# Kernel tuning notes

Hardware: AMD Instinct MI355X
Metric: run time of the kernel (lower is better)

## Reference

```python
import jax, jax.numpy as jnp
import numpy as np

B, N, C, H = 2, 2048, 1024, 16
D = C // H  # head_dim = 64

def setup_inputs() -> dict:
    key = jax.random.key(0)
    ks = jax.random.split(key, 8)
    x = jax.random.normal(ks[0], (B, N, C), jnp.float32)
    mask = jax.random.uniform(ks[1], (H, N, N), jnp.float32)
    gamma = jax.random.uniform(ks[2], (H,), jnp.float32)  # per-head decay in (0,1)
    state_prev = jax.random.normal(ks[3], (B, H, D, D), jnp.float32)
    w_scale = 0.02
    W_qkv = jax.random.normal(ks[4], (C, 3 * C), jnp.float32) * w_scale
    b_qkv = jnp.zeros((3 * C,), jnp.float32)
    W_out = jax.random.normal(ks[5], (C, C), jnp.float32) * w_scale
    b_out = jnp.zeros((C,), jnp.float32)
    return dict(x=x, mask=mask, gamma=gamma, state_prev=state_prev,
                W_qkv=W_qkv, b_qkv=b_qkv, W_out=W_out, b_out=b_out)

def reference(x, mask, gamma, state_prev, W_qkv, b_qkv, W_out, b_out):
    # Retention.chunkwise with state_prev (mode='chunkwise')
    b, n, c = x.shape
    h = gamma.shape[0]
    d = c // h
    scale = d ** -0.5
    qkv = (x @ W_qkv + b_qkv).reshape(b, n, 3, h, d)
    q = qkv[:, :, 0].transpose(0, 2, 1, 3) * scale  # [B,H,N,D]
    k = qkv[:, :, 1].transpose(0, 2, 1, 3)
    v = qkv[:, :, 2].transpose(0, 2, 1, 3)
    # intra-chunk decay-masked retention: [B,H,N,N]
    ret = jnp.einsum('bhnd,bhmd->bhnm', q, k) * mask
    ret = jnp.einsum('bhnm,bhmd->bhnd', ret, v)  # [B,H,N,D]
    inner_pos = jnp.arange(1, n + 1, dtype=x.dtype)  # [N], 1-based positions
    # state = sum_n gamma^(N-n) * k_n^T v_n (no [B,H,N,D,D] materialization)
    state_decays = gamma[:, None] ** (n - inner_pos)[None, :]  # [H,N]
    state = jnp.einsum('bhnd,bhne,hn->bhde', k, v, state_decays)  # [B,H,D,D]
    chunk_decay = gamma ** n  # [H]
    state = state + state_prev * chunk_decay[None, :, None, None]
    # cross-chunk retention against previous state
    cross = jnp.einsum('bhnd,bhde->bhne', q, state_prev)
    cross = cross * (gamma[None, :, None, None] ** inner_pos[None, None, :, None])
    ret = (ret + cross).transpose(0, 2, 1, 3).reshape(b, n, c)
    out = ret @ W_out + b_out
    return (out, state)
```

## Files before the change

kernel.cpp:

```cpp
#include <hip/hip_runtime.h>
#include <hip/hip_bf16.h>
#include <cstdint>

#define DI __device__ __forceinline__

typedef __attribute__((ext_vector_type(8))) short v8s;
typedef __attribute__((ext_vector_type(4))) float v4f;

constexpr int Bc = 2, Nc = 2048, Cc = 1024, Hc = 16, Dc = 64;

DI float bfbits(uint32_t u) { union { uint32_t i; float f; } c; c.i = u; return c.f; }
DI unsigned short f2bf(float f) {
    union { float f; uint32_t u; } c; c.f = f;
    uint32_t r = c.u + 0x7FFFu + ((c.u >> 16) & 1u);
    return (unsigned short)(r >> 16);
}
DI void unpackb8(uint4 u, float* f) {
    f[0] = bfbits(u.x << 16); f[1] = bfbits(u.x & 0xFFFF0000u);
    f[2] = bfbits(u.y << 16); f[3] = bfbits(u.y & 0xFFFF0000u);
    f[4] = bfbits(u.z << 16); f[5] = bfbits(u.z & 0xFFFF0000u);
    f[6] = bfbits(u.w << 16); f[7] = bfbits(u.w & 0xFFFF0000u);
}
DI float gpow(float g, float p) {
    if (p <= 0.f) return 1.f;
    if (g <= 0.f) return 0.f;
    return exp2f(p * log2f(g));
}

__global__ __launch_bounds__(256) void cvt_bf16(
    const float* __restrict__ in, unsigned short* __restrict__ out, int n8)
{
    int i = blockIdx.x * 256 + threadIdx.x;
    if (i >= n8) return;
    float4 a = ((const float4*)in)[i * 2];
    float4 b = ((const float4*)in)[i * 2 + 1];
    ushort4 r0; r0.x = f2bf(a.x); r0.y = f2bf(a.y); r0.z = f2bf(a.z); r0.w = f2bf(a.w);
    ushort4 r1; r1.x = f2bf(b.x); r1.y = f2bf(b.y); r1.z = f2bf(b.z); r1.w = f2bf(b.w);
    ((ushort4*)out)[i * 2] = r0; ((ushort4*)out)[i * 2 + 1] = r1;
}

__global__ __launch_bounds__(256) void transpose_cvt(
    const float* __restrict__ in, unsigned short* __restrict__ out, int R, int C)
{
    __shared__ float T[64][65];
    const int tid = threadIdx.x;
    const int r0 = blockIdx.y * 64, c0 = blockIdx.x * 64;
    #pragma unroll
    for (int rep = 0; rep < 4; rep++) {
        int row = (tid >> 4) + rep * 16, col = (tid & 15) * 4;
        float4 v = *reinterpret_cast<const float4*>(in + (size_t)(r0 + row) * C + c0 + col);
        T[row][col] = v.x; T[row][col + 1] = v.y; T[row][col + 2] = v.z; T[row][col + 3] = v.w;
    }
    __syncthreads();
    #pragma unroll
    for (int rep = 0; rep < 4; rep++) {
        int ocr = (tid >> 4) + rep * 16, j4 = (tid & 15) * 4;
        ushort4 w;
        w.x = f2bf(T[j4][ocr]);     w.y = f2bf(T[j4 + 1][ocr]);
        w.z = f2bf(T[j4 + 2][ocr]); w.w = f2bf(T[j4 + 3][ocr]);
        *reinterpret_cast<ushort4*>(out + (size_t)(c0 + ocr) * R + r0 + j4) = w;
    }
}

__global__ __launch_bounds__(256) void transpose_v(
    const unsigned short* __restrict__ in, unsigned short* __restrict__ out)
{
    __shared__ unsigned short T[64][72];
    const int tid = threadIdx.x;
    const int n0 = blockIdx.x * 64;
    const int bh = blockIdx.y;
    const unsigned short* src = in + ((size_t)bh * Nc + n0) * Dc;
    #pragma unroll
    for (int rep = 0; rep < 2; rep++) {
        int r = (tid >> 3) + rep * 32, c = (tid & 7) * 8;
        *(uint4*)&T[r][c] = *(const uint4*)(src + (size_t)r * Dc + c);
    }
    __syncthreads();
    unsigned short* dst = out + (size_t)bh * Dc * Nc + n0;
    #pragma unroll
    for (int rep = 0; rep < 2; rep++) {
        int d = (tid >> 3) + rep * 32, c0 = (tid & 7) * 8;
        union { uint4 u; unsigned short s[8]; } w;
        #pragma unroll
        for (int j = 0; j < 8; j++) w.s[j] = T[c0 + j][d];
        *(uint4*)(dst + (size_t)d * Nc + c0) = w.u;
    }
}

__global__ __launch_bounds__(256) void qkv_mfma(
    const unsigned short* __restrict__ A, const unsigned short* __restrict__ Bt,
    const float* __restrict__ bias,
    unsigned short* __restrict__ q, unsigned short* __restrict__ k,
    unsigned short* __restrict__ v)
{
    __shared__ unsigned short As[128][72];
    __shared__ unsigned short Bs[128][72];
    const int tid = threadIdx.x, wave = tid >> 6, lane = tid & 63;
    const int L = lane & 15, quad = lane >> 4;
    const int wr = (wave >> 1) * 64, wc = (wave & 1) * 64;
    const int row0 = blockIdx.y * 128, col0 = blockIdx.x * 128;
    v4f acc[4][4];
    #pragma unroll
    for (int i = 0; i < 4; i++)
        #pragma unroll
        for (int j = 0; j < 4; j++) { acc[i][j][0]=0.f; acc[i][j][1]=0.f; acc[i][j][2]=0.f; acc[i][j][3]=0.f; }
    for (int k0 = 0; k0 < 1024; k0 += 64) {
        __syncthreads();
        #pragma unroll
        for (int rep = 0; rep < 4; rep++) {
            int r = (tid >> 3) + rep * 32, cg = (tid & 7) * 8;
            *(uint4*)&As[r][cg] = *(const uint4*)(A  + (size_t)(row0 + r) * 1024 + k0 + cg);
            *(uint4*)&Bs[r][cg] = *(const uint4*)(Bt + (size_t)(col0 + r) * 1024 + k0 + cg);
        }
        __syncthreads();
        #pragma unroll
        for (int half = 0; half < 2; half++) {
            v8s af[4], bf[4];
            #pragma unroll
            for (int s = 0; s < 4; s++) {
                af[s] = *(v8s*)&As[wr + s * 16 + L][half * 32 + quad * 8];
                bf[s] = *(v8s*)&Bs[wc + s * 16 + L][half * 32 + quad * 8];
            }
            #pragma unroll
            for (int i = 0; i < 4; i++)
                #pragma unroll
                for (int j = 0; j < 4; j++)
                    acc[i][j] = __builtin_amdgcn_mfma_f32_16x16x32_bf16(af[i], bf[j], acc[i][j], 0, 0, 0);
        }
    }
    const int which = col0 >> 10;
    #pragma unroll
    for (int j = 0; j < 4; j++) {
        int c = col0 + wc + j * 16 + L;
        int h = (c & 1023) >> 6, d = c & 63;
        float bv = bias[c];
        #pragma unroll
        for (int i = 0; i < 4; i++) {
            #pragma unroll
            for (int reg = 0; reg < 4; reg++) {
                int rr = row0 + wr + i * 16 + quad * 4 + reg;
                int b = rr >> 11, n = rr & 2047;
                float val = acc[i][j][reg] + bv;
                size_t base = (((size_t)(b * Hc + h)) * Nc + n) * Dc + d;
                if (which == 0)      q[base] = f2bf(val * 0.125f);
                else if (which == 1) k[base] = f2bf(val);
                else                 v[base] = f2bf(val);
            }
        }
    }
}

__global__ __launch_bounds__(256, 4) void retention_mfma(
    const unsigned short* __restrict__ qb, const unsigned short* __restrict__ kb,
    const unsigned short* __restrict__ vtb,
    const float* __restrict__ mask, const float* __restrict__ gamma,
    const float* __restrict__ sprev,
    unsigned short* __restrict__ retb, float* __restrict__ pf0, float* __restrict__ pf1)
{
    __shared__ unsigned short Kt[64][72];
    __shared__ unsigned short Vt[64][72];
    __shared__ unsigned short Sm[64][72];
    const int tid = threadIdx.x, wave = tid >> 6, lane = tid & 63;
    const int L = lane & 15, quad = lane >> 4;
    const int h = blockIdx.y;
    const int n0 = blockIdx.x * 128;
    const int batch = blockIdx.z >> 1;
    const int chunk = blockIdx.z & 1;
    const int m_base = chunk * 1024;
    const float g = gamma[h];
    const int bh = batch * Hc + h;

    {
        #pragma unroll
        for (int rep = 0; rep < 2; rep++) {
            int r = (tid >> 3) + rep * 32, ch = (tid & 7) * 8;
            *(uint4*)&Kt[r][ch] = *(const uint4*)(qb + ((size_t)bh * Nc + n0 + r) * Dc + ch);
            *(uint4*)&Vt[r][ch] = *(const uint4*)(qb + ((size_t)bh * Nc + n0 + 64 + r) * Dc + ch);
        }
    }
    __syncthreads();
    v8s qf[2][2];
    qf[0][0] = *(v8s*)&Kt[wave * 16 + L][quad * 8];
    qf[0][1] = *(v8s*)&Kt[wave * 16 + L][32 + quad * 8];
    qf[1][0] = *(v8s*)&Vt[wave * 16 + L][quad * 8];
    qf[1][1] = *(v8s*)&Vt[wave * 16 + L][32 + quad * 8];

    v4f oacc[2][4];
    #pragma unroll
    for (int band = 0; band < 2; band++)
        #pragma unroll
        for (int s = 0; s < 4; s++) { oacc[band][s][0]=0.f; oacc[band][s][1]=0.f; oacc[band][s][2]=0.f; oacc[band][s][3]=0.f; }

    if (chunk == 0) {
        __syncthreads();
        {
            int dd = tid >> 2, e0 = (tid & 3) * 16;
            const float* sp = sprev + ((size_t)bh * 64 + dd) * 64 + e0;
            #pragma unroll
            for (int j = 0; j < 16; j++) Kt[e0 + j][dd] = f2bf(sp[j]);
        }
        __syncthreads();
        #pragma unroll
        for (int band = 0; band < 2; band++) {
            #pragma unroll
            for (int s = 0; s < 4; s++) {
                v4f a = oacc[band][s];
                a = __builtin_amdgcn_mfma_f32_16x16x32_bf16(qf[band][0], *(v8s*)&Kt[s * 16 + L][quad * 8], a, 0, 0, 0);
                a = __builtin_amdgcn_mfma_f32_16x16x32_bf16(qf[band][1], *(v8s*)&Kt[s * 16 + L][32 + quad * 8], a, 0, 0, 0);
                oacc[band][s] = a;
            }
            float cf = gpow(g, (float)(n0 + band * 64 + wave * 16 + quad * 4 + 1));
            #pragma unroll
            for (int reg = 0; reg < 4; reg++) {
                #pragma unroll
                for (int s = 0; s < 4; s++) oacc[band][s][reg] *= cf;
                cf *= g;
            }
        }
    }

    const unsigned short* kp = kb + (size_t)bh * Nc * Dc;
    const unsigned short* vt = vtb + (size_t)bh * Dc * Nc;
    const float* mbase = mask + (size_t)h * Nc * Nc;

    for (int it = 0; it < 16; ++it) {
        const int m0 = m_base + it * 64;
        __syncthreads();
        {
            #pragma unroll
            for (int rep = 0; rep < 2; rep++) {
                int r = (tid >> 3) + rep * 32, ch = (tid & 7) * 8;
                *(uint4*)&Kt[r][ch] = *(const uint4*)(kp + (size_t)(m0 + r) * Dc + ch);
                *(uint4*)&Vt[r][ch] = *(const uint4*)(vt + (size_t)r * Nc + m0 + ch);
            }
        }
        __syncthreads();
        #pragma unroll
        for (int band = 0; band < 2; band++) {
            float mv[4][4];
            #pragma unroll
            for (int s = 0; s < 4; s++)
                #pragma unroll
                for (int reg = 0; reg < 4; reg++)
                    mv[s][reg] = mbase[(size_t)(n0 + band * 64 + wave * 16 + quad * 4 + reg) * Nc + m0 + s * 16 + L];
            v4f sa[4];
            #pragma unroll
            for (int s = 0; s < 4; s++) {
                v4f a; a[0] = 0.f; a[1] = 0.f; a[2] = 0.f; a[3] = 0.f;
                a = __builtin_amdgcn_mfma_f32_16x16x32_bf16(qf[band][0], *(v8s*)&Kt[s * 16 + L][quad * 8], a, 0, 0, 0);
                a = __builtin_amdgcn_mfma_f32_16x16x32_bf16(qf[band][1], *(v8s*)&Kt[s * 16 + L][32 + quad * 8], a, 0, 0, 0);
                sa[s] = a;
            }
            #pragma unroll
            for (int s = 0; s < 4; s++)
                #pragma unroll
                for (int reg = 0; reg < 4; reg++)
                    Sm[wave * 16 + quad * 4 + reg][s * 16 + L] = f2bf(sa[s][reg] * mv[s][reg]);
            v8s af0 = *(v8s*)&Sm[wave * 16 + L][quad * 8];
            v8s af1 = *(v8s*)&Sm[wave * 16 + L][32 + quad * 8];
            #pragma unroll
            for (int s = 0; s < 4; s++) {
                oacc[band][s] = __builtin_amdgcn_mfma_f32_16x16x32_bf16(af0, *(v8s*)&Vt[s * 16 + L][quad * 8], oacc[band][s], 0, 0, 0);
                oacc[band][s] = __builtin_amdgcn_mfma_f32_16x16x32_bf16(af1, *(v8s*)&Vt[s * 16 + L][32 + quad * 8], oacc[band][s], 0, 0, 0);
            }
        }
    }

    if (chunk == 0) {
        #pragma unroll
        for (int band = 0; band < 2; band++)
            #pragma unroll
            for (int s = 0; s < 4; s++)
                #pragma unroll
                for (int reg = 0; reg < 4; reg++) {
                    int n = n0 + band * 64 + wave * 16 + quad * 4 + reg;
                    retb[((size_t)batch * Nc + n) * Cc + h * 64 + s * 16 + L] = f2bf(oacc[band][s][reg]);
                }
    } else {
        float* pd = batch ? pf1 : pf0;
        #pragma unroll
        for (int band = 0; band < 2; band++)
            #pragma unroll
            for (int s = 0; s < 4; s++)
                #pragma unroll
                for (int reg = 0; reg < 4; reg++) {
                    int n = n0 + band * 64 + wave * 16 + quad * 4 + reg;
                    pd[(size_t)n * Cc + h * 64 + s * 16 + L] = oacc[band][s][reg];
                }
    }
}

__global__ __launch_bounds__(256) void add_partial(
    unsigned short* __restrict__ retb,
    const float* __restrict__ pf0, const float* __restrict__ pf1, int n8)
{
    int i = blockIdx.x * 256 + threadIdx.x;
    if (i >= n8) return;
    int e = i * 8;
    const float* pf = (e & (1 << 21)) ? pf1 : pf0;
    const float4* pp = (const float4*)(pf + (e & ((1 << 21) - 1)));
    uint4 a = ((const uint4*)retb)[i];
    float fa[8]; unpackb8(a, fa);
    float4 x0 = pp[0], x1 = pp[1];
    ushort4 r0, r1;
    r0.x = f2bf(fa[0] + x0.x); r0.y = f2bf(fa[1] + x0.y);
    r0.z = f2bf(fa[2] + x0.z); r0.w = f2bf(fa[3] + x0.w);
    r1.x = f2bf(fa[4] + x1.x); r1.y = f2bf(fa[5] + x1.y);
    r1.z = f2bf(fa[6] + x1.z); r1.w = f2bf(fa[7] + x1.w);
    ((ushort4*)retb)[2 * i] = r0; ((ushort4*)retb)[2 * i + 1] = r1;
}

__global__ __launch_bounds__(256) void state_partial(
    const unsigned short* __restrict__ kg, const unsigned short* __restrict__ vg,
    const float* __restrict__ gamma,
    float* __restrict__ partial)
{
    __shared__ float Ks[64][65];
    __shared__ float Vs[64][65];
    __shared__ float wdec[64];
    const int chunk = blockIdx.x;
    const int bh = blockIdx.y;
    const int h = bh & 15;
    const int tid = threadIdx.x;
    const int d = tid >> 2;
    const int e0 = (tid & 3) * 16;
    const float g = gamma[h];
    const unsigned short* kbp = kg + (size_t)bh * Nc * Dc;
    const unsigned short* vbp = vg + (size_t)bh * Nc * Dc;
    float acc[16] = {};
    const int nStart = chunk * 256;
    for (int m0 = nStart; m0 < nStart + 256; m0 += 64) {
        __syncthreads();
        {
            uint4 u0 = *(const uint4*)(kbp + (size_t)(m0 + d) * 64 + e0);
            uint4 u1 = *(const uint4*)(kbp + (size_t)(m0 + d) * 64 + e0 + 8);
            float f[8];
            unpackb8(u0, f);
            #pragma unroll
            for (int j = 0; j < 8; j++) Ks[d][e0 + j] = f[j];
            unpackb8(u1, f);
            #pragma unroll
            for (int j = 0; j < 8; j++) Ks[d][e0 + 8 + j] = f[j];
            uint4 w0 = *(const uint4*)(vbp + (size_t)(m0 + d) * 64 + e0);
            uint4 w1 = *(const uint4*)(vbp + (size_t)(m0 + d) * 64 + e0 + 8);
            unpackb8(w0, f);
            #pragma unroll
            for (int j = 0; j < 8; j++) Vs[d][e0 + j] = f[j];
            unpackb8(w1, f);
            #pragma unroll
            for (int j = 0; j < 8; j++) Vs[d][e0 + 8 + j] = f[j];
        }
        if (tid < 64) wdec[tid] = gpow(g, (float)(2047 - (m0 + tid)));
        __syncthreads();
        for (int nn = 0; nn < 64; nn++) {
            float kw = Ks[nn][d] * wdec[nn];
            #pragma unroll
            for (int j = 0; j < 16; j++) acc[j] += kw * Vs[nn][e0 + j];
        }
    }
    float* pp = partial + (size_t)chunk * (Bc * Hc * Dc * Dc)
              + ((size_t)bh * 64 + d) * 64 + e0;
    #pragma unroll
    for (int j = 0; j < 16; j++) pp[j] = acc[j];
}

__global__ __launch_bounds__(256) void state_reduce(
    const float* __restrict__ partial,
    const float* __restrict__ sprev,
    const float* __restrict__ gamma,
    float* __restrict__ outState)
{
    const int idx = blockIdx.x * 256 + threadIdx.x;
    const int bh = idx >> 12;
    const int h = bh & 15;
    const float g = gamma[h];
    float acc = sprev[idx] * gpow(g, 2048.f);
    #pragma unroll
    for (int c = 0; c < 8; c++) acc += partial[(size_t)c * (Bc * Hc * Dc * Dc) + idx];
    outState[idx] = acc;
}

__global__ __launch_bounds__(256) void out_mfma(
    const unsigned short* __restrict__ A, const unsigned short* __restrict__ Bt,
    const float* __restrict__ bias,
    float* __restrict__ out)
{
    __shared__ unsigned short As[128][72];
    __shared__ unsigned short Bs[128][72];
    const int tid = threadIdx.x, wave = tid >> 6, lane = tid & 63;
    const int L = lane & 15, quad = lane >> 4;
    const int wr = (wave >> 1) * 64, wc = (wave & 1) * 64;
    const int row0 = blockIdx.y * 128, col0 = blockIdx.x * 128;
    v4f acc[4][4];
    #pragma unroll
    for (int i = 0; i < 4; i++)
        #pragma unroll
        for (int j = 0; j < 4; j++) { acc[i][j][0]=0.f; acc[i][j][1]=0.f; acc[i][j][2]=0.f; acc[i][j][3]=0.f; }
    for (int k0 = 0; k0 < 1024; k0 += 64) {
        __syncthreads();
        #pragma unroll
        for (int rep = 0; rep < 4; rep++) {
            int r = (tid >> 3) + rep * 32, cg = (tid & 7) * 8;
            *(uint4*)&As[r][cg] = *(const uint4*)(A  + (size_t)(row0 + r) * 1024 + k0 + cg);
            *(uint4*)&Bs[r][cg] = *(const uint4*)(Bt + (size_t)(col0 + r) * 1024 + k0 + cg);
        }
        __syncthreads();
        #pragma unroll
        for (int half = 0; half < 2; half++) {
            v8s af[4], bf[4];
            #pragma unroll
            for (int s = 0; s < 4; s++) {
                af[s] = *(v8s*)&As[wr + s * 16 + L][half * 32 + quad * 8];
                bf[s] = *(v8s*)&Bs[wc + s * 16 + L][half * 32 + quad * 8];
            }
            #pragma unroll
            for (int i = 0; i < 4; i++)
                #pragma unroll
                for (int j = 0; j < 4; j++)
                    acc[i][j] = __builtin_amdgcn_mfma_f32_16x16x32_bf16(af[i], bf[j], acc[i][j], 0, 0, 0);
        }
    }
    #pragma unroll
    for (int j = 0; j < 4; j++) {
        int c = col0 + wc + j * 16 + L;
        float bv = bias[c];
        #pragma unroll
        for (int i = 0; i < 4; i++) {
            #pragma unroll
            for (int reg = 0; reg < 4; reg++) {
                int rr = row0 + wr + i * 16 + quad * 4 + reg;
                out[(size_t)rr * 1024 + c] = acc[i][j][reg] + bv;
            }
        }
    }
}

extern "C" void kernel_launch(void* const* d_in, const int* in_sizes, int n_in,
                              void* d_out, int out_size, void* d_ws, size_t ws_size,
                              hipStream_t stream) {
    (void)in_sizes; (void)n_in; (void)out_size; (void)ws_size;
    const float* x     = (const float*)d_in[0];
    const float* mask  = (const float*)d_in[1];
    const float* gamma = (const float*)d_in[2];
    const float* sprev = (const float*)d_in[3];
    const float* Wqkv  = (const float*)d_in[4];
    const float* bqkv  = (const float*)d_in[5];
    const float* Wout  = (const float*)d_in[6];
    const float* bout  = (const float*)d_in[7];

    char* W = (char*)d_ws;
    unsigned short* qb   = (unsigned short*)(W);
    unsigned short* kb   = (unsigned short*)(W + 8388608);
    unsigned short* vb   = (unsigned short*)(W + 16777216);
    float*          pf0  = (float*)        (W + 16777216);
    unsigned short* retb = (unsigned short*)(W + 25165824);
    unsigned short* wot  = (unsigned short*)(W + 33554432);
    float*          part = (float*)        (W + 35651584);
    unsigned short* xb   = (unsigned short*)(W + 39845888);
    unsigned short* vtb  = (unsigned short*)(W + 39845888);
    unsigned short* wqt  = (unsigned short*)(W + 48234496);
    float*          pf1  = (float*)        (W + 54525952);

    float* out      = (float*)d_out;
    float* outState = (float*)d_out + (size_t)Bc * Nc * Cc;

    cvt_bf16<<<2048, 256, 0, stream>>>(x, xb, 524288);
    transpose_cvt<<<dim3(48, 16), 256, 0, stream>>>(Wqkv, wqt, 1024, 3072);
    transpose_cvt<<<dim3(16, 16), 256, 0, stream>>>(Wout, wot, 1024, 1024);
    qkv_mfma<<<dim3(24, 32), 256, 0, stream>>>(xb, wqt, bqkv, qb, kb, vb);
    transpose_v<<<dim3(32, 32), 256, 0, stream>>>(vb, vtb);
    state_partial<<<dim3(8, 32), 256, 0, stream>>>(kb, vb, gamma, part);
    state_reduce<<<512, 256, 0, stream>>>(part, sprev, gamma, outState);
    retention_mfma<<<dim3(16, 16, 4), 256, 0, stream>>>(qb, kb, vtb, mask, gamma, sprev,
                                                        retb, pf0, pf1);
    add_partial<<<2048, 256, 0, stream>>>(retb, pf0, pf1, 524288);
    out_mfma<<<dim3(8, 32), 256, 0, stream>>>(retb, wot, bout, out);
}
```

Before: 551.4 us.

## Fuse partial-sum add into output GEMM and use direct global-to-LDS loads

Removes the add_partial kernel by having the output projection GEMM load the bf16 retention rows plus fp32 partials, add them, and convert while filling its A tile. The qkv and output GEMMs also switch weight/input tile staging to global_load_lds direct-to-LDS copies with unpadded shared arrays. This saves a kernel launch and a round trip of the retention buffer, but the fp32 partials are now re-read by every column block, and the unpadded LDS layout may add bank conflicts on the fragment reads.

```diff
diff --git a/kernel.cpp b/kernel.cpp
--- a/kernel.cpp
+++ b/kernel.cpp
@@ -25,6 +25,12 @@
     if (p <= 0.f) return 1.f;
     if (g <= 0.f) return 0.f;
     return exp2f(p * log2f(g));
+}
+
+typedef __attribute__((address_space(3))) uint32_t as3_u32;
+typedef __attribute__((address_space(1))) uint32_t as1_u32;
+DI void gload16(const void* g, void* l) {
+    __builtin_amdgcn_global_load_lds((const as1_u32*)g, (as3_u32*)l, 16, 0, 0);
 }
 
 __global__ __launch_bounds__(256) void cvt_bf16(
@@ -93,12 +99,14 @@
     unsigned short* __restrict__ q, unsigned short* __restrict__ k,
     unsigned short* __restrict__ v)
 {
-    __shared__ unsigned short As[128][72];
-    __shared__ unsigned short Bs[128][72];
+    __shared__ unsigned short As[128][64];
+    __shared__ unsigned short Bs[128][64];
     const int tid = threadIdx.x, wave = tid >> 6, lane = tid & 63;
     const int L = lane & 15, quad = lane >> 4;
     const int wr = (wave >> 1) * 64, wc = (wave & 1) * 64;
     const int row0 = blockIdx.y * 128, col0 = blockIdx.x * 128;
+    const int srow = wave * 32 + (lane >> 3);
+    const int scol = (lane & 7) * 8;
     v4f acc[4][4];
     #pragma unroll
     for (int i = 0; i < 4; i++)
@@ -107,10 +115,9 @@
     for (int k0 = 0; k0 < 1024; k0 += 64) {
         __syncthreads();
         #pragma unroll
-        for (int rep = 0; rep < 4; rep++) {
-            int r = (tid >> 3) + rep * 32, cg = (tid & 7) * 8;
-            *(uint4*)&As[r][cg] = *(const uint4*)(A  + (size_t)(row0 + r) * 1024 + k0 + cg);
-            *(uint4*)&Bs[r][cg] = *(const uint4*)(Bt + (size_t)(col0 + r) * 1024 + k0 + cg);
+        for (int i = 0; i < 4; i++) {
+            gload16(A  + (size_t)(row0 + srow + i * 8) * 1024 + k0 + scol, &As[wave * 32 + i * 8][0]);
+            gload16(Bt + (size_t)(col0 + srow + i * 8) * 1024 + k0 + scol, &Bs[wave * 32 + i * 8][0]);
         }
         __syncthreads();
         #pragma unroll
@@ -288,26 +295,6 @@
                     pd[(size_t)n * Cc + h * 64 + s * 16 + L] = oacc[band][s][reg];
                 }
     }
-}
-
-__global__ __launch_bounds__(256) void add_partial(
-    unsigned short* __restrict__ retb,
-    const float* __restrict__ pf0, const float* __restrict__ pf1, int n8)
-{
-    int i = blockIdx.x * 256 + threadIdx.x;
-    if (i >= n8) return;
-    int e = i * 8;
-    const float* pf = (e & (1 << 21)) ? pf1 : pf0;
-    const float4* pp = (const float4*)(pf + (e & ((1 << 21) - 1)));
-    uint4 a = ((const uint4*)retb)[i];
-    float fa[8]; unpackb8(a, fa);
-    float4 x0 = pp[0], x1 = pp[1];
-    ushort4 r0, r1;
-    r0.x = f2bf(fa[0] + x0.x); r0.y = f2bf(fa[1] + x0.y);
-    r0.z = f2bf(fa[2] + x0.z); r0.w = f2bf(fa[3] + x0.w);
-    r1.x = f2bf(fa[4] + x1.x); r1.y = f2bf(fa[5] + x1.y);
-    r1.z = f2bf(fa[6] + x1.z); r1.w = f2bf(fa[7] + x1.w);
-    ((ushort4*)retb)[2 * i] = r0; ((ushort4*)retb)[2 * i + 1] = r1;
 }
 
 __global__ __launch_bounds__(256) void state_partial(
@@ -381,16 +368,20 @@
 }
 
 __global__ __launch_bounds__(256) void out_mfma(
-    const unsigned short* __restrict__ A, const unsigned short* __restrict__ Bt,
+    const unsigned short* __restrict__ Ar,
+    const float* __restrict__ pf0, const float* __restrict__ pf1,
+    const unsigned short* __restrict__ Bt,
     const float* __restrict__ bias,
     float* __restrict__ out)
 {
     __shared__ unsigned short As[128][72];
-    __shared__ unsigned short Bs[128][72];
+    __shared__ unsigned short Bs[128][64];
     const int tid = threadIdx.x, wave = tid >> 6, lane = tid & 63;
     const int L = lane & 15, quad = lane >> 4;
     const int wr = (wave >> 1) * 64, wc = (wave & 1) * 64;
     const int row0 = blockIdx.y * 128, col0 = blockIdx.x * 128;
+    const int srow = wave * 32 + (lane >> 3);
+    const int scol = (lane & 7) * 8;
     v4f acc[4][4];
     #pragma unroll
     for (int i = 0; i < 4; i++)
@@ -399,10 +390,24 @@
     for (int k0 = 0; k0 < 1024; k0 += 64) {
         __syncthreads();
         #pragma unroll
+        for (int i = 0; i < 4; i++)
+            gload16(Bt + (size_t)(col0 + srow + i * 8) * 1024 + k0 + scol, &Bs[wave * 32 + i * 8][0]);
+        #pragma unroll
         for (int rep = 0; rep < 4; rep++) {
             int r = (tid >> 3) + rep * 32, cg = (tid & 7) * 8;
-            *(uint4*)&As[r][cg] = *(const uint4*)(A  + (size_t)(row0 + r) * 1024 + k0 + cg);
-            *(uint4*)&Bs[r][cg] = *(const uint4*)(Bt + (size_t)(col0 + r) * 1024 + k0 + cg);
+            int rr = row0 + r;
+            uint4 a = *(const uint4*)(Ar + (size_t)rr * 1024 + k0 + cg);
+            const float* pf = (rr & 2048) ? pf1 : pf0;
+            const float4* pp = (const float4*)(pf + (size_t)(rr & 2047) * 1024 + k0 + cg);
+            float fa[8]; unpackb8(a, fa);
+            float4 x0 = pp[0], x1 = pp[1];
+            ushort4 w0, w1;
+            w0.x = f2bf(fa[0] + x0.x); w0.y = f2bf(fa[1] + x0.y);
+            w0.z = f2bf(fa[2] + x0.z); w0.w = f2bf(fa[3] + x0.w);
+            w1.x = f2bf(fa[4] + x1.x); w1.y = f2bf(fa[5] + x1.y);
+            w1.z = f2bf(fa[6] + x1.z); w1.w = f2bf(fa[7] + x1.w);
+            *(ushort4*)&As[r][cg] = w0;
+            *(ushort4*)&As[r][cg + 4] = w1;
         }
         __syncthreads();
         #pragma unroll
@@ -473,6 +478,5 @@
     state_reduce<<<512, 256, 0, stream>>>(part, sprev, gamma, outState);
     retention_mfma<<<dim3(16, 16, 4), 256, 0, stream>>>(qb, kb, vtb, mask, gamma, sprev,
                                                         retb, pf0, pf1);
-    add_partial<<<2048, 256, 0, stream>>>(retb, pf0, pf1, 524288);
-    out_mfma<<<dim3(8, 32), 256, 0, stream>>>(retb, wot, bout, out);
-}
+    out_mfma<<<dim3(8, 32), 256, 0, stream>>>(retb, pf0, pf1, wot, bout, out);
+}
```

Result: slower. 573.4 us (+4.0%).
